# Performance work log

Measured on AMD Instinct MI355X. Metric: run time of the kernel, lower is better.

The kernel has to match this reference:

```python
import jax, jax.numpy as jnp
import numpy as np

EPS = 1e-5
G = 8    # groups
K = 3    # kernel_size


def bn(x, gamma, beta, mean, var):
    # inference-mode BatchNorm2d; x: (b,C,H,W), params: (C,)
    inv = gamma / jnp.sqrt(var + EPS)
    return x * inv[None, :, None, None] + (beta - mean * inv)[None, :, None, None]


def gconv1x1(x, w):
    # grouped 1x1 conv; x: (b, g*ci, H, W), w: (g, co, ci) -> (b, g*co, H, W)
    b, C, H, W = x.shape
    g, co, ci = w.shape
    xg = x.reshape(b, g, ci, H, W)
    y = jnp.einsum('bgihw,goi->bgohw', xg, w)
    return y.reshape(b, g * co, H, W)


def unfold3(x):
    # torch.nn.Unfold(k=3, stride=1, dilation=1, padding=1), reshaped to (b, C, 9, H, W)
    b, C, H, W = x.shape
    xp = jnp.pad(x, ((0, 0), (0, 0), (1, 1), (1, 1)))
    patches = [xp[:, :, i:i + H, j:j + W] for i in range(K) for j in range(K)]
    return jnp.stack(patches, axis=2)


def setup_inputs() -> dict:
    key = jax.random.key(0)
    ks = jax.random.split(key, 16)
    f = jax.random.normal
    u = jax.random.uniform
    return {
        'x':  f(ks[0], (2, 256, 128, 128), jnp.float32),
        'w1': f(ks[1], (8, 8, 32), jnp.float32) * 0.1,
        'b1': f(ks[2], (64,), jnp.float32) * 0.1,
        'g1': u(ks[3], (64,), jnp.float32, 0.5, 1.5),
        'be1': f(ks[4], (64,), jnp.float32) * 0.1,
        'm1': f(ks[5], (64,), jnp.float32) * 0.1,
        'v1': u(ks[6], (64,), jnp.float32, 0.5, 1.5),
        'w2': f(ks[7], (8, 10, 8), jnp.float32) * 0.1,
        'b2': f(ks[8], (80,), jnp.float32) * 0.1,
        'g2': u(ks[9], (80,), jnp.float32, 0.5, 1.5),
        'be2': f(ks[10], (80,), jnp.float32) * 0.1,
        'm2': f(ks[11], (80,), jnp.float32) * 0.1,
        'v2': u(ks[12], (80,), jnp.float32, 0.5, 1.5),
        'wv': f(ks[13], (8, 32, 32), jnp.float32) * 0.1,
    }


def reference(x, w1, b1, g1, be1, m1, v1, w2, b2, g2, be2, m2, v2, wv):
    b, C, H, W = x.shape
    # mask_conv: grouped 1x1 conv -> BN -> tanh -> grouped 1x1 conv -> BN
    t = jnp.tanh(bn(gconv1x1(x, w1) + b1[None, :, None, None], g1, be1, m1, v1))
    mn = bn(gconv1x1(t, w2) + b2[None, :, None, None], g2, be2, m2, v2)  # (b, G*(1+K*K), H, W)
    neighbor = mn[:, :G]          # (b, G, H, W)
    mask = mn[:, G:]              # (b, G*K*K, H, W)
    nb = unfold3(neighbor)        # (b, G, 9, H, W)
    logits = mask.reshape(b, G, K * K, H, W) + nb
    attn = jax.nn.softmax(logits, axis=2)               # (b, G, 9, H, W)
    # value path: grouped 1x1 conv (no bias) then unfold
    v = gconv1x1(x, wv)                                  # (b, C, H, W)
    vu = unfold3(v).reshape(b, G, C // G, K * K, H, W)   # (b, G, C/G, 9, H, W)
    out = jnp.einsum('bgkhw,bgckhw->bgchw', attn, vu)    # weighted sum over window
    return out.reshape(b, C, H, W)
```

## Files before the change

### kernel.cpp

```cpp
#include <hip/hip_runtime.h>
#include <hip/hip_bf16.h>

#define HW  16384
#define WD  128
#define MNS 16448

#define TS   16
#define HS   18
#define HP   (HS * HS)
#define PRS  20
#define PLS  360

__device__ __forceinline__ unsigned short f2bf(float f) {
    unsigned int u = __builtin_bit_cast(unsigned int, f);
    u += 0x7FFFu + ((u >> 16) & 1u);
    return (unsigned short)(u >> 16);
}
__device__ __forceinline__ float bf2f(unsigned short s) {
    return __builtin_bit_cast(float, (unsigned int)s << 16);
}

__global__ __launch_bounds__(256) void la_k1(
    const float* __restrict__ x,
    const float* __restrict__ w1, const float* __restrict__ b1,
    const float* __restrict__ g1, const float* __restrict__ be1,
    const float* __restrict__ m1, const float* __restrict__ v1,
    const float* __restrict__ w2, const float* __restrict__ b2,
    const float* __restrict__ g2, const float* __restrict__ be2,
    const float* __restrict__ m2, const float* __restrict__ v2,
    unsigned short* __restrict__ mn)
{
    const int pix = blockIdx.x * blockDim.x + threadIdx.x;
    const int bg  = blockIdx.y;
    const int b   = bg >> 3, g = bg & 7;

    const float* xp = x + (size_t)(b * 256 + g * 32) * HW + pix;
    float xg[32];
#pragma unroll
    for (int c = 0; c < 32; ++c) xg[c] = xp[(size_t)c * HW];

    float t[8];
    const float* w1g = w1 + g * 256;
#pragma unroll
    for (int o = 0; o < 8; ++o) {
        float a = 0.f;
#pragma unroll
        for (int ci = 0; ci < 32; ++ci) a = fmaf(xg[ci], w1g[o * 32 + ci], a);
        const int ch = g * 8 + o;
        const float inv = g1[ch] * rsqrtf(v1[ch] + 1e-5f);
        const float add = be1[ch] + (b1[ch] - m1[ch]) * inv;
        t[o] = tanhf(fmaf(a, inv, add));
    }

    const float* w2g = w2 + g * 80;
    unsigned short* mnp = mn + (size_t)(b * 80 + g * 10) * MNS + pix;
#pragma unroll
    for (int o = 0; o < 10; ++o) {
        float a = 0.f;
#pragma unroll
        for (int i = 0; i < 8; ++i) a = fmaf(t[i], w2g[o * 8 + i], a);
        const int ch = g * 10 + o;
        const float inv = g2[ch] * rsqrtf(v2[ch] + 1e-5f);
        const float add = be2[ch] + (b2[ch] - m2[ch]) * inv;
        mnp[(size_t)o * MNS] = f2bf(fmaf(a, inv, add));
    }
}

__global__ __launch_bounds__(256) void la_k2(
    const float* __restrict__ x, const float* __restrict__ wv,
    const unsigned short* __restrict__ mn, float* __restrict__ out)
{
    __shared__ ushort4 vt[8 * PLS];

    const int tid  = threadIdx.x;
    const int bg   = blockIdx.x;
    const int tile = blockIdx.y;
    const int b    = bg >> 3, g = bg & 7;
    const int ty0  = (tile >> 3) * TS;
    const int tx0  = (tile & 7) * TS;

    const float* xg  = x  + (size_t)(b * 256 + g * 32) * HW;
    const float* wvg = wv + g * 1024;

    for (int hp = tid; hp < HP; hp += 256) {
        const int hy = hp / HS, hx = hp - hy * HS;
        const int iy = ty0 + hy - 1, ix = tx0 + hx - 1;
        const int slot = hy * PRS + hx;
        if (((unsigned)iy < 128u) && ((unsigned)ix < 128u)) {
            const float* xp = xg + iy * WD + ix;
            float xv[32];
#pragma unroll
            for (int c = 0; c < 32; ++c) xv[c] = xp[(size_t)c * HW];
#pragma unroll
            for (int o4 = 0; o4 < 8; ++o4) {
                float a0 = 0.f, a1 = 0.f, a2 = 0.f, a3 = 0.f;
                const float* wp = wvg + o4 * 128;
#pragma unroll
                for (int c = 0; c < 32; ++c) {
                    const float xc = xv[c];
                    a0 = fmaf(xc, wp[c],      a0);
                    a1 = fmaf(xc, wp[32 + c], a1);
                    a2 = fmaf(xc, wp[64 + c], a2);
                    a3 = fmaf(xc, wp[96 + c], a3);
                }
                vt[o4 * PLS + slot] = make_ushort4(f2bf(a0), f2bf(a1), f2bf(a2), f2bf(a3));
            }
        } else {
            const ushort4 z = make_ushort4(0, 0, 0, 0);
#pragma unroll
            for (int o4 = 0; o4 < 8; ++o4) vt[o4 * PLS + slot] = z;
        }
    }
    __syncthreads();

    const int cy  = tid >> 4, cx = tid & 15;
    const int iy  = ty0 + cy, ix = tx0 + cx;
    const int pix = iy * WD + ix;

    const unsigned short* nbp = mn + (size_t)(b * 80 + g) * MNS;
    const unsigned short* mkp = mn + (size_t)(b * 80 + 8 + g * 9) * MNS + pix;

    float lg[9];
    float mx = -1e30f;
#pragma unroll
    for (int k = 0; k < 9; ++k) {
        const int dy = k / 3 - 1, dx = k % 3 - 1;
        const int ny = iy + dy, nx = ix + dx;
        const bool ok = ((unsigned)ny < 128u) && ((unsigned)nx < 128u);
        const float nb = ok ? bf2f(nbp[ny * WD + nx]) : 0.f;
        lg[k] = bf2f(mkp[(size_t)k * MNS]) + nb;
        mx = fmaxf(mx, lg[k]);
    }
    float s = 0.f;
#pragma unroll
    for (int k = 0; k < 9; ++k) { lg[k] = __expf(lg[k] - mx); s += lg[k]; }
    const float rs = 1.f / s;
#pragma unroll
    for (int k = 0; k < 9; ++k) lg[k] *= rs;

    float* og = out + (size_t)(b * 256 + g * 32) * HW + pix;
#pragma unroll 2
    for (int o4 = 0; o4 < 8; ++o4) {
        const ushort4* vp = vt + o4 * PLS;
        float a0 = 0.f, a1 = 0.f, a2 = 0.f, a3 = 0.f;
#pragma unroll
        for (int k = 0; k < 9; ++k) {
            const int slot = (cy + k / 3) * PRS + (cx + k % 3);
            const ushort4 vv = vp[slot];
            a0 = fmaf(lg[k], bf2f(vv.x), a0);
            a1 = fmaf(lg[k], bf2f(vv.y), a1);
            a2 = fmaf(lg[k], bf2f(vv.z), a2);
            a3 = fmaf(lg[k], bf2f(vv.w), a3);
        }
        __builtin_nontemporal_store(a0, og + (size_t)(o4 * 4 + 0) * HW);
        __builtin_nontemporal_store(a1, og + (size_t)(o4 * 4 + 1) * HW);
        __builtin_nontemporal_store(a2, og + (size_t)(o4 * 4 + 2) * HW);
        __builtin_nontemporal_store(a3, og + (size_t)(o4 * 4 + 3) * HW);
    }
}

extern "C" void kernel_launch(void* const* d_in, const int* in_sizes, int n_in,
                              void* d_out, int out_size, void* d_ws, size_t ws_size,
                              hipStream_t stream)
{
    const float* x   = (const float*)d_in[0];
    const float* w1  = (const float*)d_in[1];
    const float* b1  = (const float*)d_in[2];
    const float* g1  = (const float*)d_in[3];
    const float* be1 = (const float*)d_in[4];
    const float* m1  = (const float*)d_in[5];
    const float* v1  = (const float*)d_in[6];
    const float* w2  = (const float*)d_in[7];
    const float* b2  = (const float*)d_in[8];
    const float* g2  = (const float*)d_in[9];
    const float* be2 = (const float*)d_in[10];
    const float* m2  = (const float*)d_in[11];
    const float* v2  = (const float*)d_in[12];
    const float* wv  = (const float*)d_in[13];

    float* out = (float*)d_out;
    unsigned short* mn = (unsigned short*)d_ws;

    dim3 blk(256);
    dim3 g1d(HW / 256, 16);
    dim3 g2d(16, 64);

    hipLaunchKernelGGL(la_k1, g1d, blk, 0, stream,
                       x, w1, b1, g1, be1, m1, v1, w2, b2, g2, be2, m2, v2, mn);
    hipLaunchKernelGGL(la_k2, g2d, blk, 0, stream, x, wv, mn, out);
}
```

Before: 134.1 us.

## Fuse mask-conv kernel into attention kernel, recomputing mask and neighbor logits per tile

```diff
diff --git a/kernel.cpp b/kernel.cpp
--- a/kernel.cpp
+++ b/kernel.cpp
@@ -3,7 +3,6 @@
 
 #define HW  16384
 #define WD  128
-#define MNS 16448
 
 #define TS   16
 #define HS   18
@@ -19,8 +18,12 @@
 __device__ __forceinline__ float bf2f(unsigned short s) {
     return __builtin_bit_cast(float, (unsigned int)s << 16);
 }
-
-__global__ __launch_bounds__(256) void la_k1(
+__device__ __forceinline__ float ftanh(float v) {
+    const float e = __expf(2.0f * v);
+    return 1.0f - __fdividef(2.0f, e + 1.0f);
+}
+
+__global__ __launch_bounds__(256) void la_fused(
     const float* __restrict__ x,
     const float* __restrict__ w1, const float* __restrict__ b1,
     const float* __restrict__ g1, const float* __restrict__ be1,
@@ -28,49 +31,11 @@
     const float* __restrict__ w2, const float* __restrict__ b2,
     const float* __restrict__ g2, const float* __restrict__ be2,
     const float* __restrict__ m2, const float* __restrict__ v2,
-    unsigned short* __restrict__ mn)
-{
-    const int pix = blockIdx.x * blockDim.x + threadIdx.x;
-    const int bg  = blockIdx.y;
-    const int b   = bg >> 3, g = bg & 7;
-
-    const float* xp = x + (size_t)(b * 256 + g * 32) * HW + pix;
-    float xg[32];
-#pragma unroll
-    for (int c = 0; c < 32; ++c) xg[c] = xp[(size_t)c * HW];
-
-    float t[8];
-    const float* w1g = w1 + g * 256;
-#pragma unroll
-    for (int o = 0; o < 8; ++o) {
-        float a = 0.f;
-#pragma unroll
-        for (int ci = 0; ci < 32; ++ci) a = fmaf(xg[ci], w1g[o * 32 + ci], a);
-        const int ch = g * 8 + o;
-        const float inv = g1[ch] * rsqrtf(v1[ch] + 1e-5f);
-        const float add = be1[ch] + (b1[ch] - m1[ch]) * inv;
-        t[o] = tanhf(fmaf(a, inv, add));
-    }
-
-    const float* w2g = w2 + g * 80;
-    unsigned short* mnp = mn + (size_t)(b * 80 + g * 10) * MNS + pix;
-#pragma unroll
-    for (int o = 0; o < 10; ++o) {
-        float a = 0.f;
-#pragma unroll
-        for (int i = 0; i < 8; ++i) a = fmaf(t[i], w2g[o * 8 + i], a);
-        const int ch = g * 10 + o;
-        const float inv = g2[ch] * rsqrtf(v2[ch] + 1e-5f);
-        const float add = be2[ch] + (b2[ch] - m2[ch]) * inv;
-        mnp[(size_t)o * MNS] = f2bf(fmaf(a, inv, add));
-    }
-}
-
-__global__ __launch_bounds__(256) void la_k2(
-    const float* __restrict__ x, const float* __restrict__ wv,
-    const unsigned short* __restrict__ mn, float* __restrict__ out)
+    const float* __restrict__ wv,
+    float* __restrict__ out)
 {
     __shared__ ushort4 vt[8 * PLS];
+    __shared__ float   nbs[PLS];
 
     const int tid  = threadIdx.x;
     const int bg   = blockIdx.x;
@@ -79,18 +44,25 @@
     const int ty0  = (tile >> 3) * TS;
     const int tx0  = (tile & 7) * TS;
 
-    const float* xg  = x  + (size_t)(b * 256 + g * 32) * HW;
+    const float* xg  = x + (size_t)(b * 256 + g * 32) * HW;
+    const float* x0  = x + (size_t)(b * 256) * HW;
     const float* wvg = wv + g * 1024;
+
+    const float inv_nb = g2[g] * rsqrtf(v2[g] + 1e-5f);
+    const float add_nb = be2[g] + (b2[g] - m2[g]) * inv_nb;
 
     for (int hp = tid; hp < HP; hp += 256) {
         const int hy = hp / HS, hx = hp - hy * HS;
         const int iy = ty0 + hy - 1, ix = tx0 + hx - 1;
         const int slot = hy * PRS + hx;
         if (((unsigned)iy < 128u) && ((unsigned)ix < 128u)) {
-            const float* xp = xg + iy * WD + ix;
-            float xv[32];
-#pragma unroll
-            for (int c = 0; c < 32; ++c) xv[c] = xp[(size_t)c * HW];
+            const int po = iy * WD + ix;
+            float xv[32], xz[32];
+#pragma unroll
+            for (int c = 0; c < 32; ++c) xv[c] = xg[(size_t)c * HW + po];
+#pragma unroll
+            for (int c = 0; c < 32; ++c) xz[c] = x0[(size_t)c * HW + po];
+
 #pragma unroll
             for (int o4 = 0; o4 < 8; ++o4) {
                 float a0 = 0.f, a1 = 0.f, a2 = 0.f, a3 = 0.f;
@@ -105,10 +77,24 @@
                 }
                 vt[o4 * PLS + slot] = make_ushort4(f2bf(a0), f2bf(a1), f2bf(a2), f2bf(a3));
             }
+
+            float accn = 0.f;
+#pragma unroll
+            for (int o = 0; o < 8; ++o) {
+                float a = 0.f;
+#pragma unroll
+                for (int ci = 0; ci < 32; ++ci) a = fmaf(xz[ci], w1[o * 32 + ci], a);
+                const float inv = g1[o] * rsqrtf(v1[o] + 1e-5f);
+                const float add = be1[o] + (b1[o] - m1[o]) * inv;
+                const float t0 = ftanh(fmaf(a, inv, add));
+                accn = fmaf(t0, w2[g * 8 + o], accn);
+            }
+            nbs[slot] = fmaf(accn, inv_nb, add_nb);
         } else {
             const ushort4 z = make_ushort4(0, 0, 0, 0);
 #pragma unroll
             for (int o4 = 0; o4 < 8; ++o4) vt[o4 * PLS + slot] = z;
+            nbs[slot] = 0.f;
         }
     }
     __syncthreads();
@@ -117,18 +103,68 @@
     const int iy  = ty0 + cy, ix = tx0 + cx;
     const int pix = iy * WD + ix;
 
-    const unsigned short* nbp = mn + (size_t)(b * 80 + g) * MNS;
-    const unsigned short* mkp = mn + (size_t)(b * 80 + 8 + g * 9) * MNS + pix;
+    const int mc0    = 8 + 9 * g;
+    const int pa     = mc0 / 10;
+    const int pb     = (mc0 + 8) / 10;
+    const int ksplit = 10 - (mc0 - pa * 10);
+
+    float tA[8], tB[8];
+    {
+        const float* xp  = x  + (size_t)(b * 256 + pa * 32) * HW + pix;
+        const float* w1p = w1 + pa * 256;
+        float xv[32];
+#pragma unroll
+        for (int c = 0; c < 32; ++c) xv[c] = xp[(size_t)c * HW];
+#pragma unroll
+        for (int o = 0; o < 8; ++o) {
+            float a = 0.f;
+#pragma unroll
+            for (int ci = 0; ci < 32; ++ci) a = fmaf(xv[ci], w1p[o * 32 + ci], a);
+            const int ch = pa * 8 + o;
+            const float inv = g1[ch] * rsqrtf(v1[ch] + 1e-5f);
+            const float add = be1[ch] + (b1[ch] - m1[ch]) * inv;
+            tA[o] = ftanh(fmaf(a, inv, add));
+        }
+    }
+    if (pb != pa) {
+        const float* xp  = x  + (size_t)(b * 256 + pb * 32) * HW + pix;
+        const float* w1p = w1 + pb * 256;
+        float xv[32];
+#pragma unroll
+        for (int c = 0; c < 32; ++c) xv[c] = xp[(size_t)c * HW];
+#pragma unroll
+        for (int o = 0; o < 8; ++o) {
+            float a = 0.f;
+#pragma unroll
+            for (int ci = 0; ci < 32; ++ci) a = fmaf(xv[ci], w1p[o * 32 + ci], a);
+            const int ch = pb * 8 + o;
+            const float inv = g1[ch] * rsqrtf(v1[ch] + 1e-5f);
+            const float add = be1[ch] + (b1[ch] - m1[ch]) * inv;
+            tB[o] = ftanh(fmaf(a, inv, add));
+        }
+    } else {
+#pragma unroll
+        for (int o = 0; o < 8; ++o) tB[o] = tA[o];
+    }
 
     float lg[9];
     float mx = -1e30f;
 #pragma unroll
     for (int k = 0; k < 9; ++k) {
-        const int dy = k / 3 - 1, dx = k % 3 - 1;
-        const int ny = iy + dy, nx = ix + dx;
-        const bool ok = ((unsigned)ny < 128u) && ((unsigned)nx < 128u);
-        const float nb = ok ? bf2f(nbp[ny * WD + nx]) : 0.f;
-        lg[k] = bf2f(mkp[(size_t)k * MNS]) + nb;
+        const int mc = mc0 + k;
+        const int p  = (k < ksplit) ? pa : pb;
+        const int o  = mc - p * 10;
+        const float* w2p = w2 + p * 80 + o * 8;
+        float a = 0.f;
+#pragma unroll
+        for (int i = 0; i < 8; ++i) {
+            const float ti = (k < ksplit) ? tA[i] : tB[i];
+            a = fmaf(ti, w2p[i], a);
+        }
+        const float inv = g2[mc] * rsqrtf(v2[mc] + 1e-5f);
+        const float add = be2[mc] + (b2[mc] - m2[mc]) * inv;
+        const float mask = fmaf(a, inv, add);
+        lg[k] = mask + nbs[(cy + k / 3) * PRS + (cx + k % 3)];
         mx = fmaxf(mx, lg[k]);
     }
     float s = 0.f;
@@ -179,13 +215,11 @@
     const float* wv  = (const float*)d_in[13];
 
     float* out = (float*)d_out;
-    unsigned short* mn = (unsigned short*)d_ws;
 
     dim3 blk(256);
-    dim3 g1d(HW / 256, 16);
-    dim3 g2d(16, 64);
-
-    hipLaunchKernelGGL(la_k1, g1d, blk, 0, stream,
-                       x, w1, b1, g1, be1, m1, v1, w2, b2, g2, be2, m2, v2, mn);
-    hipLaunchKernelGGL(la_k2, g2d, blk, 0, stream, x, wv, mn, out);
-}
+    dim3 grd(16, 64);
+
+    hipLaunchKernelGGL(la_fused, grd, blk, 0, stream,
+                       x, w1, b1, g1, be1, m1, v1, w2, b2, g2, be2, m2, v2, wv,
+                       out);
+}
```

Result: slower. 142.0 us (+5.9%).
